# Kernel tuning notes

Hardware: AMD Instinct MI355X
Metric: run time of the kernel (lower is better)

## Reference

```python
import jax, jax.numpy as jnp
import numpy as np

WAYPOINTS_IX = jnp.array([0, 2, 4, 6, 9, 12, 15, 19])
LOG_2PI = float(np.log(2.0 * np.pi))


def setup_inputs() -> dict:
    key = jax.random.key(0)
    ks = jax.random.split(key, 5)
    bs, W, K, D = 64, 8, 10, 2
    P, T, N = 16, 20, 4096
    mu = jax.random.normal(ks[0], (bs, W, K, D), dtype=jnp.float32)
    # sigma must be strictly positive
    sigma = jax.random.uniform(ks[1], (bs, W, K, D), dtype=jnp.float32) * 0.9 + 0.1
    pi = jax.random.normal(ks[2], (bs, W, K), dtype=jnp.float32)
    negative_targets = jax.random.normal(ks[3], (bs, N, D), dtype=jnp.float32)
    positive_targets = jax.random.normal(ks[4], (bs, P, T, D), dtype=jnp.float32)
    return {
        "mu": mu,
        "sigma": sigma,
        "pi": pi,
        "negative_targets": negative_targets,
        "positive_targets": positive_targets,
        "target_is_wh": 1,
        "num_negatives_cap": 1024,
    }


def reference(mu, sigma, pi, negative_targets, positive_targets, target_is_wh, num_negatives_cap):
    bs, N, D = negative_targets.shape
    if target_is_wh:
        negative_targets = negative_targets[..., ::-1]
        positive_targets = positive_targets[..., ::-1]
    # select waypoints: [bs, P, W, 2]
    pos = positive_targets[:, :, WAYPOINTS_IX, :]
    W = pos.shape[2]

    # pairwise L2 distance positives vs negatives: [bs, P, W, N]
    diff = pos[:, :, :, None, :] - negative_targets[:, None, None, :, :]
    dist = jnp.sqrt(jnp.sum(diff * diff, axis=-1))
    # min over positive trajectories P -> [bs, W, N]
    dist = jnp.min(dist, axis=1)

    if 0 < num_negatives_cap < N:
        # k smallest distances per (bs, W)
        neg_vals, inds = jax.lax.top_k(-dist, num_negatives_cap)  # [bs, W, C]
        dist = -neg_vals
        neg_b = jnp.broadcast_to(negative_targets[:, None, :, :], (bs, W, N, D))
        neg = jnp.take_along_axis(neg_b, jnp.repeat(inds[..., None], D, axis=-1), axis=2)  # [bs, W, C, 2]
    else:
        neg = jnp.broadcast_to(negative_targets[:, None, :, :], (bs, W, N, D))

    # softmin over candidates: [bs, W, C]
    weights = jax.nn.softmax(-dist, axis=-1)

    # mixture-of-diagonal-Gaussians log prob of each negative
    # neg: [bs, W, C, 1, 2], mu/sigma: [bs, W, 1, K, 2]
    z = (neg[:, :, :, None, :] - mu[:, :, None, :, :]) / sigma[:, :, None, :, :]
    comp_lp = jnp.sum(-0.5 * z * z - jnp.log(sigma)[:, :, None, :, :] - 0.5 * LOG_2PI, axis=-1)  # [bs,W,C,K]
    log_mix = jax.nn.log_softmax(pi, axis=-1)[:, :, None, :]  # [bs,W,1,K]
    log_probs = jax.nn.logsumexp(comp_lp + log_mix, axis=-1)  # [bs, W, C]

    # weighted log prob; torch reduces mean over W then sum over C
    loss = -jnp.sum(jnp.mean(log_probs * weights, axis=1), axis=-1)  # [bs]
    return loss
```

## Files before the change

### kernel.cpp

```cpp
#include <hip/hip_runtime.h>
#include <math.h>

#define BS   64
#define NW   8
#define NK   10
#define NP   16
#define NT   20
#define NN   4096
#define NTH  512
#define NWAVES (NTH / 64)
#define EPT  (NN / NTH)
#define NBINS 4096
#define CANDMAX 2048
#define LOG2PI 1.8378770664093453f
#define LOG2E  1.4426950408889634f
#define LN2    0.6931471805599453f

__device__ __constant__ int d_wpix[NW] = {0, 2, 4, 6, 9, 12, 15, 19};

__global__ __launch_bounds__(NTH, 4) void mdn_row_kernel(
    const float* __restrict__ mu,
    const float* __restrict__ sigma,
    const float* __restrict__ pi,
    const float* __restrict__ neg,
    const float* __restrict__ pos,
    const int* __restrict__ p_wh,
    const int* __restrict__ p_cap,
    float* __restrict__ rowres)
{
    __shared__ unsigned int s_hist[NBINS];
    __shared__ unsigned int s_cand[CANDMAX];
    __shared__ float s_posx[NP], s_posy[NP];
    __shared__ float s_mu0[NK], s_mu1[NK], s_is0[NK], s_is1[NK], s_ck2[NK];
    __shared__ unsigned int s_wsum[NWAVES];
    __shared__ float s_red[2 * NWAVES];
    __shared__ unsigned int s_bucket, s_below, s_candcnt, s_P;
    __shared__ float s_dmin;

    const int row  = blockIdx.x;
    const int b    = row / NW;
    const int w    = row % NW;
    const int tid  = threadIdx.x;
    const int lane = tid & 63;
    const int wid  = tid >> 6;

    #pragma unroll
    for (int j = 0; j < NBINS / NTH; ++j) s_hist[tid + j * NTH] = 0;
    if (tid < NP) {
        const float* pp = pos + (((size_t)b * NP + tid) * NT + d_wpix[w]) * 2;
        s_posx[tid] = pp[0];
        s_posy[tid] = pp[1];
    }
    if (tid >= 64 && tid < 64 + NK) {
        const int k = tid - 64;
        const float* pib = pi    + ((size_t)b * NW + w) * NK;
        const float* mub = mu    + ((size_t)b * NW + w) * NK * 2;
        const float* sgb = sigma + ((size_t)b * NW + w) * NK * 2;
        float m = pib[0];
        for (int j = 1; j < NK; ++j) m = fmaxf(m, pib[j]);
        float se = 0.f;
        for (int j = 0; j < NK; ++j) se += __expf(pib[j] - m);
        float lse = m + __logf(se);
        float s0 = sgb[2 * k], s1 = sgb[2 * k + 1];
        s_mu0[k] = mub[2 * k];
        s_mu1[k] = mub[2 * k + 1];
        s_is0[k] = 1.0f / s0;
        s_is1[k] = 1.0f / s1;
        s_ck2[k] = ((pib[k] - lse) - __logf(s0) - __logf(s1) - LOG2PI) * LOG2E;
    }
    if (tid == 32) s_candcnt = 0;
    __syncthreads();

    float px[NP], py[NP];
    #pragma unroll
    for (int p = 0; p < NP; ++p) { px[p] = s_posx[p]; py[p] = s_posy[p]; }

    const float2* negp = (const float2*)(neg + (size_t)b * NN * 2);
    float nx[EPT], ny[EPT];
    unsigned int ub[EPT];
    float lmin = INFINITY;
    #pragma unroll
    for (int c = 0; c < EPT; ++c) {
        const int n = c * NTH + tid;
        float2 v = negp[n];
        nx[c] = v.x; ny[c] = v.y;
        float best = INFINITY;
        #pragma unroll
        for (int p = 0; p < NP; ++p) {
            float dx = px[p] - v.x;
            float dy = py[p] - v.y;
            best = fminf(best, fmaf(dx, dx, dy * dy));
        }
        float dd = sqrtf(best);
        ub[c] = __float_as_uint(dd);
        lmin = fminf(lmin, dd);
        atomicAdd(&s_hist[ub[c] >> 20], 1u);
    }
    #pragma unroll
    for (int off = 32; off; off >>= 1) lmin = fminf(lmin, __shfl_down(lmin, off, 64));
    if (lane == 0) s_red[wid] = lmin;
    __syncthreads();
    if (tid == 0) {
        float m = s_red[0];
        for (int i = 1; i < NWAVES; ++i) m = fminf(m, s_red[i]);
        s_dmin = m;
    }

    const int cap = *p_cap;
    const bool do_sel = (cap > 0 && cap < NN);
    const int wh = *p_wh;

    float accZ = 0.f, accS = 0.f;

    if (do_sel) {
        const int base = tid * (NBINS / NTH);
        unsigned int hv[NBINS / NTH];
        unsigned int cnt = 0;
        #pragma unroll
        for (int j = 0; j < NBINS / NTH; ++j) { hv[j] = s_hist[base + j]; cnt += hv[j]; }
        unsigned int v = cnt;
        #pragma unroll
        for (int off = 1; off < 64; off <<= 1) {
            unsigned int o = __shfl_up(v, off, 64);
            if (lane >= off) v += o;
        }
        if (lane == 63) s_wsum[wid] = v;
        __syncthreads();
        unsigned int wbase = 0;
        for (int i = 0; i < wid; ++i) wbase += s_wsum[i];
        const unsigned int incl = v + wbase;
        const unsigned int excl = incl - cnt;
        const unsigned int capu = (unsigned int)cap;
        if (excl < capu && capu <= incl) {
            unsigned int run = excl;
            #pragma unroll
            for (int j = 0; j < NBINS / NTH; ++j) {
                unsigned int c2 = hv[j];
                if (capu <= run + c2) { s_bucket = (unsigned int)(base + j); s_below = run; break; }
                run += c2;
            }
        }
        __syncthreads();
        const unsigned int B = s_bucket;

        #pragma unroll
        for (int c = 0; c < EPT; ++c) {
            if ((ub[c] >> 20) == B) {
                unsigned int p0 = atomicAdd(&s_candcnt, 1u);
                if (p0 < CANDMAX)
                    s_cand[p0] = (ub[c] << 12) | (unsigned int)(c * NTH + tid);
            }
        }
        __syncthreads();

        const int C = (int)min(s_candcnt, (unsigned int)CANDMAX);
        const int remT = cap - (int)s_below;
        for (int i = tid; i < C; i += NTH) {
            unsigned int pv = s_cand[i];
            int less = 0;
            for (int j = 0; j < C; ++j) less += (s_cand[j] < pv) ? 1 : 0;
            if (less == remT - 1) s_P = pv;
        }
        __syncthreads();
        const unsigned int P = s_P;

        int cs = 0;
        bool selv[EPT];
        #pragma unroll
        for (int c = 0; c < EPT; ++c) {
            const unsigned int u = ub[c];
            const unsigned int top = u >> 20;
            bool s = (top < B) ||
                     (top == B && (((u << 12) | (unsigned int)(c * NTH + tid)) <= P));
            selv[c] = s;
            cs += s ? 1 : 0;
        }
        unsigned int v2 = (unsigned int)cs;
        #pragma unroll
        for (int off = 1; off < 64; off <<= 1) {
            unsigned int o = __shfl_up(v2, off, 64);
            if (lane >= off) v2 += o;
        }
        if (lane == 63) s_wsum[wid] = v2;
        __syncthreads();
        unsigned int wb2 = 0;
        for (int i = 0; i < wid; ++i) wb2 += s_wsum[i];
        int wpos = (int)(v2 + wb2) - cs;
        const float dmin = s_dmin;
        float* selx = (float*)&s_hist[0];
        float* sely = (float*)&s_hist[1024];
        float* sele = (float*)&s_hist[2048];
        #pragma unroll
        for (int c = 0; c < EPT; ++c) {
            if (selv[c]) {
                float dd = __uint_as_float(ub[c]);
                selx[wpos] = wh ? ny[c] : nx[c];
                sely[wpos] = wh ? nx[c] : ny[c];
                sele[wpos] = exp2f((dmin - dd) * LOG2E);
                ++wpos;
            }
        }
        __syncthreads();

        for (int i = tid; i < cap; i += NTH) {
            const float x0 = selx[i], x1 = sely[i], e = sele[i];
            float a[NK];
            float m2 = -INFINITY;
            #pragma unroll
            for (int k = 0; k < NK; ++k) {
                float z0 = (x0 - s_mu0[k]) * s_is0[k];
                float z1 = (x1 - s_mu1[k]) * s_is1[k];
                float q  = fmaf(z0, z0, z1 * z1);
                float ak = fmaf(q, -0.5f * LOG2E, s_ck2[k]);
                a[k] = ak;
                m2 = fmaxf(m2, ak);
            }
            float se = 0.f;
            #pragma unroll
            for (int k = 0; k < NK; ++k) se += exp2f(a[k] - m2);
            float lp = LN2 * (m2 + log2f(se));
            accZ += e;
            accS += e * lp;
        }
    } else {
        __syncthreads();
        const float dmin = s_dmin;
        #pragma unroll
        for (int c = 0; c < EPT; ++c) {
            const float x0 = wh ? ny[c] : nx[c];
            const float x1 = wh ? nx[c] : ny[c];
            const float dd = __uint_as_float(ub[c]);
            const float e  = exp2f((dmin - dd) * LOG2E);
            float a[NK];
            float m2 = -INFINITY;
            #pragma unroll
            for (int k = 0; k < NK; ++k) {
                float z0 = (x0 - s_mu0[k]) * s_is0[k];
                float z1 = (x1 - s_mu1[k]) * s_is1[k];
                float q  = fmaf(z0, z0, z1 * z1);
                float ak = fmaf(q, -0.5f * LOG2E, s_ck2[k]);
                a[k] = ak;
                m2 = fmaxf(m2, ak);
            }
            float se = 0.f;
            #pragma unroll
            for (int k = 0; k < NK; ++k) se += exp2f(a[k] - m2);
            float lp = LN2 * (m2 + log2f(se));
            accZ += e;
            accS += e * lp;
        }
    }

    #pragma unroll
    for (int off = 32; off; off >>= 1) {
        accZ += __shfl_down(accZ, off, 64);
        accS += __shfl_down(accS, off, 64);
    }
    if (lane == 0) { s_red[wid] = accZ; s_red[NWAVES + wid] = accS; }
    __syncthreads();
    if (tid == 0) {
        float Z = 0.f, S = 0.f;
        for (int i = 0; i < NWAVES; ++i) { Z += s_red[i]; S += s_red[NWAVES + i]; }
        rowres[row] = S / Z;
    }
}

__global__ void mdn_finalize_kernel(const float* __restrict__ rowres,
                                    float* __restrict__ out)
{
    int b = threadIdx.x;
    if (b < BS) {
        float s = 0.f;
        #pragma unroll
        for (int w = 0; w < NW; ++w) s += rowres[b * NW + w];
        out[b] = -s * (1.0f / NW);
    }
}

extern "C" void kernel_launch(void* const* d_in, const int* in_sizes, int n_in,
                              void* d_out, int out_size, void* d_ws, size_t ws_size,
                              hipStream_t stream)
{
    const float* mu    = (const float*)d_in[0];
    const float* sigma = (const float*)d_in[1];
    const float* pi    = (const float*)d_in[2];
    const float* neg   = (const float*)d_in[3];
    const float* pos   = (const float*)d_in[4];
    const int*   wh    = (const int*)d_in[5];
    const int*   cap   = (const int*)d_in[6];
    float* rowres = (float*)d_ws;
    float* out    = (float*)d_out;

    mdn_row_kernel<<<BS * NW, NTH, 0, stream>>>(mu, sigma, pi, neg, pos, wh, cap, rowres);
    mdn_finalize_kernel<<<1, 64, 0, stream>>>(rowres, out);
}
```

Baseline: 21.50 us.

## Fuse finalize into row kernel, wave-local compaction, ballot atomics, padded histogram

Several changes at once. The finalize kernel is folded into the row kernel through a per-batch atomic counter and last-block reduction, with a memset added before the launch. Selected negatives are compacted into per-wave shared segments using ballot and mbcnt, which removes one block-wide scan and barrier. Candidate insertion uses one atomic per wave, the histogram is padded to spread LDS bank conflicts, loads are issued earlier, and the Gaussian parameters are cached in registers. The costs are more shared memory, which may lower occupancy, and an extra memset launch.

```diff
diff --git a/kernel.cpp b/kernel.cpp
--- a/kernel.cpp
+++ b/kernel.cpp
@@ -11,12 +11,19 @@
 #define NWAVES (NTH / 64)
 #define EPT  (NN / NTH)
 #define NBINS 4096
+#define HISTPAD (NBINS + NBINS / 8)
 #define CANDMAX 2048
+#define SEGCAP 512
 #define LOG2PI 1.8378770664093453f
 #define LOG2E  1.4426950408889634f
 #define LN2    0.6931471805599453f
 
 __device__ __constant__ int d_wpix[NW] = {0, 2, 4, 6, 9, 12, 15, 19};
+
+__device__ __forceinline__ unsigned int lanes_below(unsigned long long m) {
+    unsigned int lt = __builtin_amdgcn_mbcnt_lo((unsigned int)m, 0u);
+    return __builtin_amdgcn_mbcnt_hi((unsigned int)(m >> 32), lt);
+}
 
 __global__ __launch_bounds__(NTH, 4) void mdn_row_kernel(
     const float* __restrict__ mu,
@@ -26,10 +33,13 @@
     const float* __restrict__ pos,
     const int* __restrict__ p_wh,
     const int* __restrict__ p_cap,
-    float* __restrict__ rowres)
+    float* __restrict__ rowres,
+    unsigned int* __restrict__ cnt,
+    float* __restrict__ out)
 {
-    __shared__ unsigned int s_hist[NBINS];
+    __shared__ unsigned int s_hist[HISTPAD];
     __shared__ unsigned int s_cand[CANDMAX];
+    __shared__ float s_seg[3 * NWAVES * SEGCAP];
     __shared__ float s_posx[NP], s_posy[NP];
     __shared__ float s_mu0[NK], s_mu1[NK], s_is0[NK], s_is1[NK], s_ck2[NK];
     __shared__ unsigned int s_wsum[NWAVES];
@@ -44,8 +54,11 @@
     const int lane = tid & 63;
     const int wid  = tid >> 6;
 
-    #pragma unroll
-    for (int j = 0; j < NBINS / NTH; ++j) s_hist[tid + j * NTH] = 0;
+    const float2* negp = (const float2*)(neg + (size_t)b * NN * 2);
+    float2 nv[EPT];
+    #pragma unroll
+    for (int c = 0; c < EPT; ++c) nv[c] = negp[c * NTH + tid];
+
     if (tid < NP) {
         const float* pp = pos + (((size_t)b * NP + tid) * NT + d_wpix[w]) * 2;
         s_posx[tid] = pp[0];
@@ -68,6 +81,7 @@
         s_is1[k] = 1.0f / s1;
         s_ck2[k] = ((pib[k] - lse) - __logf(s0) - __logf(s1) - LOG2PI) * LOG2E;
     }
+    for (int i = tid; i < HISTPAD; i += NTH) s_hist[i] = 0;
     if (tid == 32) s_candcnt = 0;
     __syncthreads();
 
@@ -75,26 +89,25 @@
     #pragma unroll
     for (int p = 0; p < NP; ++p) { px[p] = s_posx[p]; py[p] = s_posy[p]; }
 
-    const float2* negp = (const float2*)(neg + (size_t)b * NN * 2);
     float nx[EPT], ny[EPT];
     unsigned int ub[EPT];
     float lmin = INFINITY;
     #pragma unroll
     for (int c = 0; c < EPT; ++c) {
-        const int n = c * NTH + tid;
-        float2 v = negp[n];
-        nx[c] = v.x; ny[c] = v.y;
-        float best = INFINITY;
-        #pragma unroll
-        for (int p = 0; p < NP; ++p) {
-            float dx = px[p] - v.x;
-            float dy = py[p] - v.y;
-            best = fminf(best, fmaf(dx, dx, dy * dy));
-        }
-        float dd = sqrtf(best);
+        nx[c] = nv[c].x; ny[c] = nv[c].y;
+        float best0 = INFINITY, best1 = INFINITY;
+        #pragma unroll
+        for (int p = 0; p < NP; p += 2) {
+            float dx0 = px[p] - nx[c],     dy0 = py[p] - ny[c];
+            float dx1 = px[p + 1] - nx[c], dy1 = py[p + 1] - ny[c];
+            best0 = fminf(best0, fmaf(dx0, dx0, dy0 * dy0));
+            best1 = fminf(best1, fmaf(dx1, dx1, dy1 * dy1));
+        }
+        float dd = sqrtf(fminf(best0, best1));
         ub[c] = __float_as_uint(dd);
         lmin = fminf(lmin, dd);
-        atomicAdd(&s_hist[ub[c] >> 20], 1u);
+        unsigned int h = ub[c] >> 20;
+        atomicAdd(&s_hist[h + (h >> 3)], 1u);
     }
     #pragma unroll
     for (int off = 32; off; off >>= 1) lmin = fminf(lmin, __shfl_down(lmin, off, 64));
@@ -110,15 +123,15 @@
     const bool do_sel = (cap > 0 && cap < NN);
     const int wh = *p_wh;
 
-    float accZ = 0.f, accS = 0.f;
+    unsigned int selmask = 0xFFu;
 
     if (do_sel) {
-        const int base = tid * (NBINS / NTH);
-        unsigned int hv[NBINS / NTH];
-        unsigned int cnt = 0;
-        #pragma unroll
-        for (int j = 0; j < NBINS / NTH; ++j) { hv[j] = s_hist[base + j]; cnt += hv[j]; }
-        unsigned int v = cnt;
+        const int rbase = tid * 9;
+        unsigned int hv[8];
+        unsigned int cnt8 = 0;
+        #pragma unroll
+        for (int j = 0; j < 8; ++j) { hv[j] = s_hist[rbase + j]; cnt8 += hv[j]; }
+        unsigned int v = cnt8;
         #pragma unroll
         for (int off = 1; off < 64; off <<= 1) {
             unsigned int o = __shfl_up(v, off, 64);
@@ -129,14 +142,14 @@
         unsigned int wbase = 0;
         for (int i = 0; i < wid; ++i) wbase += s_wsum[i];
         const unsigned int incl = v + wbase;
-        const unsigned int excl = incl - cnt;
+        const unsigned int excl = incl - cnt8;
         const unsigned int capu = (unsigned int)cap;
         if (excl < capu && capu <= incl) {
             unsigned int run = excl;
             #pragma unroll
-            for (int j = 0; j < NBINS / NTH; ++j) {
+            for (int j = 0; j < 8; ++j) {
                 unsigned int c2 = hv[j];
-                if (capu <= run + c2) { s_bucket = (unsigned int)(base + j); s_below = run; break; }
+                if (capu <= run + c2) { s_bucket = (unsigned int)(tid * 8 + j); s_below = run; break; }
                 run += c2;
             }
         }
@@ -145,10 +158,18 @@
 
         #pragma unroll
         for (int c = 0; c < EPT; ++c) {
-            if ((ub[c] >> 20) == B) {
-                unsigned int p0 = atomicAdd(&s_candcnt, 1u);
-                if (p0 < CANDMAX)
-                    s_cand[p0] = (ub[c] << 12) | (unsigned int)(c * NTH + tid);
+            bool isc = ((ub[c] >> 20) == B);
+            unsigned long long m = __ballot(isc);
+            if (m) {
+                int leader = __builtin_ctzll(m);
+                unsigned int base2 = 0;
+                if (lane == leader) base2 = atomicAdd(&s_candcnt, (unsigned int)__popcll(m));
+                base2 = __shfl(base2, leader, 64);
+                if (isc) {
+                    unsigned int p0 = base2 + lanes_below(m);
+                    if (p0 < CANDMAX)
+                        s_cand[p0] = (ub[c] << 12) | (unsigned int)(c * NTH + tid);
+                }
             }
         }
         __syncthreads();
@@ -164,91 +185,70 @@
         __syncthreads();
         const unsigned int P = s_P;
 
-        int cs = 0;
-        bool selv[EPT];
+        selmask = 0;
         #pragma unroll
         for (int c = 0; c < EPT; ++c) {
             const unsigned int u = ub[c];
             const unsigned int top = u >> 20;
             bool s = (top < B) ||
                      (top == B && (((u << 12) | (unsigned int)(c * NTH + tid)) <= P));
-            selv[c] = s;
-            cs += s ? 1 : 0;
-        }
-        unsigned int v2 = (unsigned int)cs;
-        #pragma unroll
-        for (int off = 1; off < 64; off <<= 1) {
-            unsigned int o = __shfl_up(v2, off, 64);
-            if (lane >= off) v2 += o;
-        }
-        if (lane == 63) s_wsum[wid] = v2;
-        __syncthreads();
-        unsigned int wb2 = 0;
-        for (int i = 0; i < wid; ++i) wb2 += s_wsum[i];
-        int wpos = (int)(v2 + wb2) - cs;
-        const float dmin = s_dmin;
-        float* selx = (float*)&s_hist[0];
-        float* sely = (float*)&s_hist[1024];
-        float* sele = (float*)&s_hist[2048];
-        #pragma unroll
-        for (int c = 0; c < EPT; ++c) {
-            if (selv[c]) {
-                float dd = __uint_as_float(ub[c]);
-                selx[wpos] = wh ? ny[c] : nx[c];
-                sely[wpos] = wh ? nx[c] : ny[c];
-                sele[wpos] = exp2f((dmin - dd) * LOG2E);
-                ++wpos;
-            }
-        }
-        __syncthreads();
-
-        for (int i = tid; i < cap; i += NTH) {
-            const float x0 = selx[i], x1 = sely[i], e = sele[i];
-            float a[NK];
-            float m2 = -INFINITY;
-            #pragma unroll
-            for (int k = 0; k < NK; ++k) {
-                float z0 = (x0 - s_mu0[k]) * s_is0[k];
-                float z1 = (x1 - s_mu1[k]) * s_is1[k];
-                float q  = fmaf(z0, z0, z1 * z1);
-                float ak = fmaf(q, -0.5f * LOG2E, s_ck2[k]);
-                a[k] = ak;
-                m2 = fmaxf(m2, ak);
-            }
-            float se = 0.f;
-            #pragma unroll
-            for (int k = 0; k < NK; ++k) se += exp2f(a[k] - m2);
-            float lp = LN2 * (m2 + log2f(se));
-            accZ += e;
-            accS += e * lp;
+            selmask |= (s ? 1u : 0u) << c;
         }
     } else {
         __syncthreads();
-        const float dmin = s_dmin;
-        #pragma unroll
-        for (int c = 0; c < EPT; ++c) {
-            const float x0 = wh ? ny[c] : nx[c];
-            const float x1 = wh ? nx[c] : ny[c];
-            const float dd = __uint_as_float(ub[c]);
-            const float e  = exp2f((dmin - dd) * LOG2E);
-            float a[NK];
-            float m2 = -INFINITY;
-            #pragma unroll
-            for (int k = 0; k < NK; ++k) {
-                float z0 = (x0 - s_mu0[k]) * s_is0[k];
-                float z1 = (x1 - s_mu1[k]) * s_is1[k];
-                float q  = fmaf(z0, z0, z1 * z1);
-                float ak = fmaf(q, -0.5f * LOG2E, s_ck2[k]);
-                a[k] = ak;
-                m2 = fmaxf(m2, ak);
-            }
-            float se = 0.f;
-            #pragma unroll
-            for (int k = 0; k < NK; ++k) se += exp2f(a[k] - m2);
-            float lp = LN2 * (m2 + log2f(se));
-            accZ += e;
-            accS += e * lp;
-        }
+    }
+
+    float* segx = s_seg;
+    float* segy = s_seg + NWAVES * SEGCAP;
+    float* sege = s_seg + 2 * NWAVES * SEGCAP;
+    const int segbase = wid << 9;
+    const float dmin = s_dmin;
+    int wcnt = 0;
+    #pragma unroll
+    for (int c = 0; c < EPT; ++c) {
+        bool s = (selmask >> c) & 1u;
+        unsigned long long m = __ballot(s);
+        if (s) {
+            int p0 = segbase + wcnt + (int)lanes_below(m);
+            float dd = __uint_as_float(ub[c]);
+            segx[p0] = wh ? ny[c] : nx[c];
+            segy[p0] = wh ? nx[c] : ny[c];
+            sege[p0] = exp2f((dmin - dd) * LOG2E);
+        }
+        wcnt += (int)__popcll(m);
+    }
+    asm volatile("s_waitcnt lgkmcnt(0)" ::: "memory");
+
+    float c_mu0[NK], c_mu1[NK], c_is0[NK], c_is1[NK], c_ck2[NK];
+    #pragma unroll
+    for (int k = 0; k < NK; ++k) {
+        c_mu0[k] = s_mu0[k]; c_mu1[k] = s_mu1[k];
+        c_is0[k] = s_is0[k]; c_is1[k] = s_is1[k];
+        c_ck2[k] = s_ck2[k];
+    }
+    float accZ = 0.f, accS = 0.f;
+    for (int i = lane; i < wcnt; i += 64) {
+        const float x0 = segx[segbase + i];
+        const float x1 = segy[segbase + i];
+        const float e  = sege[segbase + i];
+        float a[NK];
+        #pragma unroll
+        for (int k = 0; k < NK; ++k) {
+            float z0 = (x0 - c_mu0[k]) * c_is0[k];
+            float z1 = (x1 - c_mu1[k]) * c_is1[k];
+            float q  = fmaf(z0, z0, z1 * z1);
+            a[k] = fmaf(q, -0.5f * LOG2E, c_ck2[k]);
+        }
+        float t0 = fmaxf(a[0], a[1]), t1 = fmaxf(a[2], a[3]);
+        float t2 = fmaxf(a[4], a[5]), t3 = fmaxf(a[6], a[7]);
+        float t4 = fmaxf(a[8], a[9]);
+        float m2 = fmaxf(fmaxf(fmaxf(t0, t1), fmaxf(t2, t3)), t4);
+        float se = 0.f;
+        #pragma unroll
+        for (int k = 0; k < NK; ++k) se += exp2f(a[k] - m2);
+        float lp = LN2 * (m2 + log2f(se));
+        accZ += e;
+        accS += e * lp;
     }
 
     #pragma unroll
@@ -262,18 +262,15 @@
         float Z = 0.f, S = 0.f;
         for (int i = 0; i < NWAVES; ++i) { Z += s_red[i]; S += s_red[NWAVES + i]; }
         rowres[row] = S / Z;
-    }
-}
-
-__global__ void mdn_finalize_kernel(const float* __restrict__ rowres,
-                                    float* __restrict__ out)
-{
-    int b = threadIdx.x;
-    if (b < BS) {
-        float s = 0.f;
-        #pragma unroll
-        for (int w = 0; w < NW; ++w) s += rowres[b * NW + w];
-        out[b] = -s * (1.0f / NW);
+        __threadfence();
+        unsigned int old = atomicAdd(&cnt[b], 1u);
+        if (old == NW - 1) {
+            __threadfence();
+            float s = 0.f;
+            #pragma unroll
+            for (int j = 0; j < NW; ++j) s += rowres[b * NW + j];
+            out[b] = -s * (1.0f / NW);
+        }
     }
 }
 
@@ -289,8 +286,9 @@
     const int*   wh    = (const int*)d_in[5];
     const int*   cap   = (const int*)d_in[6];
     float* rowres = (float*)d_ws;
+    unsigned int* cnt = (unsigned int*)((char*)d_ws + 2048);
     float* out    = (float*)d_out;
 
-    mdn_row_kernel<<<BS * NW, NTH, 0, stream>>>(mu, sigma, pi, neg, pos, wh, cap, rowres);
-    mdn_finalize_kernel<<<1, 64, 0, stream>>>(rowres, out);
+    hipMemsetAsync(cnt, 0, BS * sizeof(unsigned int), stream);
+    mdn_row_kernel<<<BS * NW, NTH, 0, stream>>>(mu, sigma, pi, neg, pos, wh, cap, rowres, cnt, out);
 }
```

Result: slower. 32.12 us (+49.4%).

## Pad histogram, aggregate candidate atomics, drop dmin reduction, split min chains

Applied to the files above, without the earlier changes.

Pads the shared histogram index to reduce bank conflicts on atomic adds and scans. Candidate appends now use one wave-level atomic per ballot plus mbcnt offsets instead of one atomic per element. The block-wide min-distance reduction and its barrier are removed, so softmin weights use exp(-d) directly without the max shift. Distance min and logsumexp max are split into parallel chains for more ILP. Dropping the shift risks underflow for large distances, which the standard normal inputs here do not reach.

```diff
diff --git a/kernel.cpp b/kernel.cpp
--- a/kernel.cpp
+++ b/kernel.cpp
@@ -11,12 +11,19 @@
 #define NWAVES (NTH / 64)
 #define EPT  (NN / NTH)
 #define NBINS 4096
+#define HP(i) ((i) + ((i) >> 3))
+#define HISTPAD (NBINS + NBINS / 8)
 #define CANDMAX 2048
 #define LOG2PI 1.8378770664093453f
 #define LOG2E  1.4426950408889634f
 #define LN2    0.6931471805599453f
 
 __device__ __constant__ int d_wpix[NW] = {0, 2, 4, 6, 9, 12, 15, 19};
+
+__device__ __forceinline__ unsigned int lanes_below(unsigned long long m) {
+    unsigned int lt = __builtin_amdgcn_mbcnt_lo((unsigned int)m, 0u);
+    return __builtin_amdgcn_mbcnt_hi((unsigned int)(m >> 32), lt);
+}
 
 __global__ __launch_bounds__(NTH, 4) void mdn_row_kernel(
     const float* __restrict__ mu,
@@ -28,14 +35,13 @@
     const int* __restrict__ p_cap,
     float* __restrict__ rowres)
 {
-    __shared__ unsigned int s_hist[NBINS];
+    __shared__ unsigned int s_hist[HISTPAD];
     __shared__ unsigned int s_cand[CANDMAX];
     __shared__ float s_posx[NP], s_posy[NP];
     __shared__ float s_mu0[NK], s_mu1[NK], s_is0[NK], s_is1[NK], s_ck2[NK];
     __shared__ unsigned int s_wsum[NWAVES];
     __shared__ float s_red[2 * NWAVES];
     __shared__ unsigned int s_bucket, s_below, s_candcnt, s_P;
-    __shared__ float s_dmin;
 
     const int row  = blockIdx.x;
     const int b    = row / NW;
@@ -44,8 +50,7 @@
     const int lane = tid & 63;
     const int wid  = tid >> 6;
 
-    #pragma unroll
-    for (int j = 0; j < NBINS / NTH; ++j) s_hist[tid + j * NTH] = 0;
+    for (int i = tid; i < HISTPAD; i += NTH) s_hist[i] = 0;
     if (tid < NP) {
         const float* pp = pos + (((size_t)b * NP + tid) * NT + d_wpix[w]) * 2;
         s_posx[tid] = pp[0];
@@ -78,33 +83,25 @@
     const float2* negp = (const float2*)(neg + (size_t)b * NN * 2);
     float nx[EPT], ny[EPT];
     unsigned int ub[EPT];
-    float lmin = INFINITY;
     #pragma unroll
     for (int c = 0; c < EPT; ++c) {
         const int n = c * NTH + tid;
         float2 v = negp[n];
         nx[c] = v.x; ny[c] = v.y;
-        float best = INFINITY;
-        #pragma unroll
-        for (int p = 0; p < NP; ++p) {
-            float dx = px[p] - v.x;
-            float dy = py[p] - v.y;
-            best = fminf(best, fmaf(dx, dx, dy * dy));
-        }
-        float dd = sqrtf(best);
+        float best0 = INFINITY, best1 = INFINITY;
+        #pragma unroll
+        for (int p = 0; p < NP; p += 2) {
+            float dx0 = px[p] - v.x,     dy0 = py[p] - v.y;
+            float dx1 = px[p + 1] - v.x, dy1 = py[p + 1] - v.y;
+            best0 = fminf(best0, fmaf(dx0, dx0, dy0 * dy0));
+            best1 = fminf(best1, fmaf(dx1, dx1, dy1 * dy1));
+        }
+        float dd = sqrtf(fminf(best0, best1));
         ub[c] = __float_as_uint(dd);
-        lmin = fminf(lmin, dd);
-        atomicAdd(&s_hist[ub[c] >> 20], 1u);
-    }
-    #pragma unroll
-    for (int off = 32; off; off >>= 1) lmin = fminf(lmin, __shfl_down(lmin, off, 64));
-    if (lane == 0) s_red[wid] = lmin;
+        unsigned int h = ub[c] >> 20;
+        atomicAdd(&s_hist[HP(h)], 1u);
+    }
     __syncthreads();
-    if (tid == 0) {
-        float m = s_red[0];
-        for (int i = 1; i < NWAVES; ++i) m = fminf(m, s_red[i]);
-        s_dmin = m;
-    }
 
     const int cap = *p_cap;
     const bool do_sel = (cap > 0 && cap < NN);
@@ -113,12 +110,12 @@
     float accZ = 0.f, accS = 0.f;
 
     if (do_sel) {
-        const int base = tid * (NBINS / NTH);
-        unsigned int hv[NBINS / NTH];
-        unsigned int cnt = 0;
-        #pragma unroll
-        for (int j = 0; j < NBINS / NTH; ++j) { hv[j] = s_hist[base + j]; cnt += hv[j]; }
-        unsigned int v = cnt;
+        const int base = tid * 8;
+        unsigned int hv[8];
+        unsigned int cnt8 = 0;
+        #pragma unroll
+        for (int j = 0; j < 8; ++j) { hv[j] = s_hist[HP(base + j)]; cnt8 += hv[j]; }
+        unsigned int v = cnt8;
         #pragma unroll
         for (int off = 1; off < 64; off <<= 1) {
             unsigned int o = __shfl_up(v, off, 64);
@@ -129,12 +126,12 @@
         unsigned int wbase = 0;
         for (int i = 0; i < wid; ++i) wbase += s_wsum[i];
         const unsigned int incl = v + wbase;
-        const unsigned int excl = incl - cnt;
+        const unsigned int excl = incl - cnt8;
         const unsigned int capu = (unsigned int)cap;
         if (excl < capu && capu <= incl) {
             unsigned int run = excl;
             #pragma unroll
-            for (int j = 0; j < NBINS / NTH; ++j) {
+            for (int j = 0; j < 8; ++j) {
                 unsigned int c2 = hv[j];
                 if (capu <= run + c2) { s_bucket = (unsigned int)(base + j); s_below = run; break; }
                 run += c2;
@@ -145,10 +142,18 @@
 
         #pragma unroll
         for (int c = 0; c < EPT; ++c) {
-            if ((ub[c] >> 20) == B) {
-                unsigned int p0 = atomicAdd(&s_candcnt, 1u);
-                if (p0 < CANDMAX)
-                    s_cand[p0] = (ub[c] << 12) | (unsigned int)(c * NTH + tid);
+            bool isc = ((ub[c] >> 20) == B);
+            unsigned long long m = __ballot(isc);
+            if (m) {
+                int leader = __builtin_ctzll(m);
+                unsigned int base2 = 0;
+                if (lane == leader) base2 = atomicAdd(&s_candcnt, (unsigned int)__popcll(m));
+                base2 = __shfl(base2, leader, 64);
+                if (isc) {
+                    unsigned int p0 = base2 + lanes_below(m);
+                    if (p0 < CANDMAX)
+                        s_cand[p0] = (ub[c] << 12) | (unsigned int)(c * NTH + tid);
+                }
             }
         }
         __syncthreads();
@@ -186,7 +191,6 @@
         unsigned int wb2 = 0;
         for (int i = 0; i < wid; ++i) wb2 += s_wsum[i];
         int wpos = (int)(v2 + wb2) - cs;
-        const float dmin = s_dmin;
         float* selx = (float*)&s_hist[0];
         float* sely = (float*)&s_hist[1024];
         float* sele = (float*)&s_hist[2048];
@@ -196,7 +200,7 @@
                 float dd = __uint_as_float(ub[c]);
                 selx[wpos] = wh ? ny[c] : nx[c];
                 sely[wpos] = wh ? nx[c] : ny[c];
-                sele[wpos] = exp2f((dmin - dd) * LOG2E);
+                sele[wpos] = exp2f(-dd * LOG2E);
                 ++wpos;
             }
         }
@@ -205,16 +209,16 @@
         for (int i = tid; i < cap; i += NTH) {
             const float x0 = selx[i], x1 = sely[i], e = sele[i];
             float a[NK];
-            float m2 = -INFINITY;
             #pragma unroll
             for (int k = 0; k < NK; ++k) {
                 float z0 = (x0 - s_mu0[k]) * s_is0[k];
                 float z1 = (x1 - s_mu1[k]) * s_is1[k];
                 float q  = fmaf(z0, z0, z1 * z1);
-                float ak = fmaf(q, -0.5f * LOG2E, s_ck2[k]);
-                a[k] = ak;
-                m2 = fmaxf(m2, ak);
-            }
+                a[k] = fmaf(q, -0.5f * LOG2E, s_ck2[k]);
+            }
+            float t0 = fmaxf(a[0], a[1]), t1 = fmaxf(a[2], a[3]);
+            float t2 = fmaxf(a[4], a[5]), t3 = fmaxf(a[6], a[7]);
+            float m2 = fmaxf(fmaxf(fmaxf(t0, t1), fmaxf(t2, t3)), fmaxf(a[8], a[9]));
             float se = 0.f;
             #pragma unroll
             for (int k = 0; k < NK; ++k) se += exp2f(a[k] - m2);
@@ -223,25 +227,22 @@
             accS += e * lp;
         }
     } else {
-        __syncthreads();
-        const float dmin = s_dmin;
         #pragma unroll
         for (int c = 0; c < EPT; ++c) {
             const float x0 = wh ? ny[c] : nx[c];
             const float x1 = wh ? nx[c] : ny[c];
-            const float dd = __uint_as_float(ub[c]);
-            const float e  = exp2f((dmin - dd) * LOG2E);
+            const float e  = exp2f(-__uint_as_float(ub[c]) * LOG2E);
             float a[NK];
-            float m2 = -INFINITY;
             #pragma unroll
             for (int k = 0; k < NK; ++k) {
                 float z0 = (x0 - s_mu0[k]) * s_is0[k];
                 float z1 = (x1 - s_mu1[k]) * s_is1[k];
                 float q  = fmaf(z0, z0, z1 * z1);
-                float ak = fmaf(q, -0.5f * LOG2E, s_ck2[k]);
-                a[k] = ak;
-                m2 = fmaxf(m2, ak);
-            }
+                a[k] = fmaf(q, -0.5f * LOG2E, s_ck2[k]);
+            }
+            float t0 = fmaxf(a[0], a[1]), t1 = fmaxf(a[2], a[3]);
+            float t2 = fmaxf(a[4], a[5]), t3 = fmaxf(a[6], a[7]);
+            float m2 = fmaxf(fmaxf(fmaxf(t0, t1), fmaxf(t2, t3)), fmaxf(a[8], a[9]));
             float se = 0.f;
             #pragma unroll
             for (int k = 0; k < NK; ++k) se += exp2f(a[k] - m2);
```

After: 22.87 us. 1.06x slower.
